# Kernel optimization log

Hardware: AMD Instinct MI355X
Metric: run time of the kernel (lower is better)

The kernel has to match this reference:

```python
import jax, jax.numpy as jnp
import numpy as np

N, E = 50000, 1600000
IN_DIM, HID, HEADS, DH, NCLS = 1280, 256, 4, 64, 6
NEG_SLOPE = 0.2
LN_EPS = 1e-5


def setup_inputs() -> dict:
    key = jax.random.key(0)
    ks = jax.random.split(key, 24)
    p = {}
    p['x'] = jax.random.normal(ks[0], (N, IN_DIM), dtype=jnp.float32)
    p['edge_index'] = jax.random.randint(ks[1], (2, E), 0, N, dtype=jnp.int64)
    s = 0.05
    p['W_in'] = jax.random.normal(ks[2], (IN_DIM, HID), dtype=jnp.float32) * s
    p['b_in'] = jnp.zeros((HID,), jnp.float32)
    for l in range(2):
        p[f'W_gat{l}'] = jax.random.normal(ks[3 + 6 * l], (HID, HEADS * DH), dtype=jnp.float32) * s
        p[f'att_src{l}'] = jax.random.normal(ks[4 + 6 * l], (HEADS, DH), dtype=jnp.float32) * s
        p[f'att_dst{l}'] = jax.random.normal(ks[5 + 6 * l], (HEADS, DH), dtype=jnp.float32) * s
        p[f'b_gat{l}'] = jnp.zeros((HEADS * DH,), jnp.float32)
        p[f'ln_g{l}'] = jnp.ones((HID,), jnp.float32)
        p[f'ln_b{l}'] = jnp.zeros((HID,), jnp.float32)
    p['W_c1'] = jax.random.normal(ks[20], (HID, HID // 2), dtype=jnp.float32) * s
    p['b_c1'] = jnp.zeros((HID // 2,), jnp.float32)
    p['W_c2'] = jax.random.normal(ks[21], (HID // 2, NCLS), dtype=jnp.float32) * s
    p['b_c2'] = jnp.zeros((NCLS,), jnp.float32)
    return p


def _layer_norm(h, g, b):
    mu = jnp.mean(h, axis=-1, keepdims=True)
    var = jnp.mean((h - mu) ** 2, axis=-1, keepdims=True)
    return (h - mu) * jax.lax.rsqrt(var + LN_EPS) * g + b


def _gat_conv(h, src, dst, W, a_src, a_dst, bias):
    # h: [N, HID] -> per-head projections [N, H, DH]
    xh = (h @ W).reshape(N, HEADS, DH)
    al_src = jnp.sum(xh * a_src, axis=-1)  # [N, H]
    al_dst = jnp.sum(xh * a_dst, axis=-1)  # [N, H]
    e = jax.nn.leaky_relu(al_src[src] + al_dst[dst], NEG_SLOPE)  # [E', H]
    # edge softmax over incoming edges of each destination node
    m = jax.ops.segment_max(e, dst, num_segments=N)
    e = jnp.exp(e - m[dst])
    denom = jax.ops.segment_sum(e, dst, num_segments=N)
    w = e / denom[dst]  # [E', H]
    msg = xh[src] * w[:, :, None]  # [E', H, DH]
    out = jax.ops.segment_sum(msg, dst, num_segments=N)  # [N, H, DH]
    return out.reshape(N, HEADS * DH) + bias


def reference(x, edge_index, W_in, b_in, W_gat0, att_src0, att_dst0, b_gat0, ln_g0, ln_b0,
              W_gat1, att_src1, att_dst1, b_gat1, ln_g1, ln_b1, W_c1, b_c1, W_c2, b_c2):
    # add self loops (PyG GATConv default)
    loop = jnp.arange(N, dtype=edge_index.dtype)
    src = jnp.concatenate([edge_index[0], loop])
    dst = jnp.concatenate([edge_index[1], loop])

    h = jax.nn.relu(x @ W_in + b_in)

    for (Wg, asrc, adst, bg, g, b) in ((W_gat0, att_src0, att_dst0, b_gat0, ln_g0, ln_b0),
                                       (W_gat1, att_src1, att_dst1, b_gat1, ln_g1, ln_b1)):
        h_new = _gat_conv(h, src, dst, Wg, asrc, adst, bg)
        h_new = jax.nn.relu(_layer_norm(h_new, g, b))
        h = h + h_new

    logits = jax.nn.relu(h @ W_c1 + b_c1) @ W_c2 + b_c2
    return logits
```

## Files before the change

### kernel.cpp

```cpp
#include <hip/hip_runtime.h>

#define NN 50000
#define EE 1600000
#define INDIM 1280
#define HID 256
#define HEADS 4
#define DHD 64
#define NCLS 6
#define NEG 0.2f
#define LNEPS 1e-5f

typedef __attribute__((ext_vector_type(8))) short short8;
typedef __attribute__((ext_vector_type(4))) float floatx4;

__device__ __forceinline__ unsigned short f2b(float f) {
    unsigned int u = __float_as_uint(f);
    u += 0x7FFF + ((u >> 16) & 1);
    return (unsigned short)(u >> 16);
}
__device__ __forceinline__ float b2f(unsigned short b) {
    return __uint_as_float(((unsigned int)b) << 16);
}

__global__ void init_cnt_kernel(int* __restrict__ cnt) {
    int n = blockIdx.x * 256 + threadIdx.x;
    if (n < NN) cnt[n] = 1;
}

__global__ void count_edges_kernel(const int* __restrict__ dst, int* __restrict__ cnt) {
    int e = blockIdx.x * 256 + threadIdx.x;
    if (e < EE) atomicAdd(&cnt[dst[e]], 1);
}

__global__ __launch_bounds__(1024) void scan1_kernel(const int* __restrict__ cnt,
                                                     int* __restrict__ scanned,
                                                     int* __restrict__ chtot, int n) {
    __shared__ int wsum[16];
    int tid = threadIdx.x, lane = tid & 63, wv = tid >> 6;
    int i = blockIdx.x * 1024 + tid;
    int s = (i < n) ? cnt[i] : 0;
#pragma unroll
    for (int off = 1; off < 64; off <<= 1) {
        int t = __shfl_up(s, off, 64);
        if (lane >= off) s += t;
    }
    if (lane == 63) wsum[wv] = s;
    __syncthreads();
    if (tid < 16) {
        int ws = wsum[tid];
#pragma unroll
        for (int off = 1; off < 16; off <<= 1) {
            int t = __shfl_up(ws, off, 16);
            if (tid >= off) ws += t;
        }
        wsum[tid] = ws;
    }
    __syncthreads();
    s += (wv > 0) ? wsum[wv - 1] : 0;
    if (i < n) scanned[i] = s;
    if (tid == 1023) chtot[blockIdx.x] = s;
}

__global__ void scan2_kernel(int* __restrict__ chtot, int nch) {
    int lane = threadIdx.x;
    int v = (lane < nch) ? chtot[lane] : 0;
#pragma unroll
    for (int off = 1; off < 64; off <<= 1) {
        int t = __shfl_up(v, off, 64);
        if (lane >= off) v += t;
    }
    if (lane < nch) chtot[lane] = v;
}

__global__ void scan3_kernel(const int* __restrict__ scanned, const int* __restrict__ chtot,
                             int* __restrict__ rowptr, int n) {
    int i = blockIdx.x * 256 + threadIdx.x;
    if (i == 0) rowptr[0] = 0;
    if (i < n) {
        int ch = i >> 10;
        rowptr[i + 1] = scanned[i] + (ch ? chtot[ch - 1] : 0);
    }
}

__global__ void copyfill_kernel(const int* __restrict__ rowptr, int* __restrict__ cursor,
                                int* __restrict__ csr) {
    int n = blockIdx.x * 256 + threadIdx.x;
    if (n < NN) {
        int p = rowptr[n];
        csr[p] = n;
        cursor[n] = p + 1;
    }
}

__global__ void scatter_edges_kernel(const int* __restrict__ src, const int* __restrict__ dst,
                                     int* __restrict__ cursor, int* __restrict__ csr) {
    int e = blockIdx.x * 256 + threadIdx.x;
    if (e < EE) {
        int d = dst[e];
        int pos = atomicAdd(&cursor[d], 1);
        csr[pos] = src[e];
    }
}

__global__ void transpose_w_kernel(const float* __restrict__ W, unsigned short* __restrict__ WT,
                                   int K, int N) {
    int idx = blockIdx.x * 256 + threadIdx.x;
    if (idx >= K * N) return;
    int n = idx / K, k = idx % K;
    WT[idx] = f2b(W[(size_t)k * N + n]);
}

template <int AF32, int ACT, int WF32, int WB16>
__global__ __launch_bounds__(256) void mgemm_kernel(const float* __restrict__ Af,
                                                    const unsigned short* __restrict__ Ab,
                                                    const unsigned short* __restrict__ BT,
                                                    const float* __restrict__ bias,
                                                    float* __restrict__ Cf,
                                                    unsigned short* __restrict__ Cb,
                                                    int M, int K, int N) {
    __shared__ __align__(16) unsigned short Als[16 * 512];
    __shared__ __align__(16) unsigned short Bls[8 * 512];
    int tid = threadIdx.x;
    int wv = tid >> 6, ln = tid & 63;
    int n0 = blockIdx.x * 64, m0 = blockIdx.y * 128;

    floatx4 acc[2][4] = {};

    for (int k0 = 0; k0 < K; k0 += 64) {
#pragma unroll
        for (int i = 0; i < 4; i++) {
            int e = tid + i * 256;
            int r = e >> 3, c8 = e & 7;
            int gm = m0 + r;
            int4 v = {0, 0, 0, 0};
            if (gm < M) {
                if (AF32) {
                    const float* s = Af + (size_t)gm * K + k0 + c8 * 8;
                    float4 f0 = *(const float4*)s;
                    float4 f1 = *(const float4*)(s + 4);
                    unsigned short u[8] = {f2b(f0.x), f2b(f0.y), f2b(f0.z), f2b(f0.w),
                                           f2b(f1.x), f2b(f1.y), f2b(f1.z), f2b(f1.w)};
                    v = *(const int4*)u;
                } else {
                    v = *(const int4*)(Ab + (size_t)gm * K + k0 + c8 * 8);
                }
            }
            int blk = (r >> 4) * 2 + (c8 >> 2);
            int lslot = (r & 15) + 16 * (c8 & 3);
            *(int4*)&Als[blk * 512 + lslot * 8] = v;
        }
#pragma unroll
        for (int i = 0; i < 2; i++) {
            int e = tid + i * 256;
            int r = e >> 3, c8 = e & 7;
            int4 v = *(const int4*)(BT + (size_t)(n0 + r) * K + k0 + c8 * 8);
            int blk = (r >> 4) * 2 + (c8 >> 2);
            int lslot = (r & 15) + 16 * (c8 & 3);
            *(int4*)&Bls[blk * 512 + lslot * 8] = v;
        }
        __syncthreads();
#pragma unroll
        for (int ks = 0; ks < 2; ks++) {
            short8 a0 = *(const short8*)&Als[((wv * 2 + 0) * 2 + ks) * 512 + ln * 8];
            short8 a1 = *(const short8*)&Als[((wv * 2 + 1) * 2 + ks) * 512 + ln * 8];
#pragma unroll
            for (int nt = 0; nt < 4; nt++) {
                short8 b = *(const short8*)&Bls[(nt * 2 + ks) * 512 + ln * 8];
                acc[0][nt] = __builtin_amdgcn_mfma_f32_16x16x32_bf16(a0, b, acc[0][nt], 0, 0, 0);
                acc[1][nt] = __builtin_amdgcn_mfma_f32_16x16x32_bf16(a1, b, acc[1][nt], 0, 0, 0);
            }
        }
        __syncthreads();
    }

#pragma unroll
    for (int ms = 0; ms < 2; ms++) {
#pragma unroll
        for (int nt = 0; nt < 4; nt++) {
            int col = n0 + nt * 16 + (ln & 15);
            int rb = m0 + (wv * 2 + ms) * 16 + (ln >> 4) * 4;
            float bi = bias ? bias[col] : 0.f;
#pragma unroll
            for (int r = 0; r < 4; r++) {
                int row = rb + r;
                if (row < M) {
                    float v = acc[ms][nt][r] + bi;
                    if (ACT) v = fmaxf(v, 0.f);
                    if (WF32) Cf[(size_t)row * N + col] = v;
                    if (WB16) Cb[(size_t)row * N + col] = f2b(v);
                }
            }
        }
    }
}

template <int AF32, int ACT, int WF32, int WB16>
__global__ __launch_bounds__(256) void mgemm_n256_kernel(const float* __restrict__ Af,
                                                         const unsigned short* __restrict__ Ab,
                                                         const unsigned short* __restrict__ BT,
                                                         const float* __restrict__ bias,
                                                         float* __restrict__ Cf,
                                                         unsigned short* __restrict__ Cb,
                                                         int M, int K) {
    __shared__ __align__(16) unsigned short Als[8 * 512];
    __shared__ __align__(16) unsigned short Bls[32 * 512];
    int tid = threadIdx.x;
    int wv = tid >> 6, ln = tid & 63;
    int m0 = blockIdx.x * 64;

    floatx4 acc[4][4] = {};

    for (int k0 = 0; k0 < K; k0 += 64) {
#pragma unroll
        for (int i = 0; i < 2; i++) {
            int e = tid + i * 256;
            int r = e >> 3, c8 = e & 7;
            int gm = m0 + r;
            int4 v = {0, 0, 0, 0};
            if (gm < M) {
                if (AF32) {
                    const float* s = Af + (size_t)gm * K + k0 + c8 * 8;
                    float4 f0 = *(const float4*)s;
                    float4 f1 = *(const float4*)(s + 4);
                    unsigned short u[8] = {f2b(f0.x), f2b(f0.y), f2b(f0.z), f2b(f0.w),
                                           f2b(f1.x), f2b(f1.y), f2b(f1.z), f2b(f1.w)};
                    v = *(const int4*)u;
                } else {
                    v = *(const int4*)(Ab + (size_t)gm * K + k0 + c8 * 8);
                }
            }
            int blk = (r >> 4) * 2 + (c8 >> 2);
            int lslot = (r & 15) + 16 * (c8 & 3);
            *(int4*)&Als[blk * 512 + lslot * 8] = v;
        }
#pragma unroll
        for (int i = 0; i < 8; i++) {
            int e = tid + i * 256;
            int r = e >> 3, c8 = e & 7;
            int4 v = *(const int4*)(BT + (size_t)r * K + k0 + c8 * 8);
            int blk = (r >> 4) * 2 + (c8 >> 2);
            int lslot = (r & 15) + 16 * (c8 & 3);
            *(int4*)&Bls[blk * 512 + lslot * 8] = v;
        }
        __syncthreads();
#pragma unroll
        for (int ks = 0; ks < 2; ks++) {
            short8 am[4];
#pragma unroll
            for (int mt = 0; mt < 4; mt++)
                am[mt] = *(const short8*)&Als[(mt * 2 + ks) * 512 + ln * 8];
#pragma unroll
            for (int nt4 = 0; nt4 < 4; nt4++) {
                int nt = wv * 4 + nt4;
                short8 b = *(const short8*)&Bls[(nt * 2 + ks) * 512 + ln * 8];
#pragma unroll
                for (int mt = 0; mt < 4; mt++)
                    acc[mt][nt4] = __builtin_amdgcn_mfma_f32_16x16x32_bf16(am[mt], b, acc[mt][nt4], 0, 0, 0);
            }
        }
        __syncthreads();
    }

#pragma unroll
    for (int mt = 0; mt < 4; mt++) {
#pragma unroll
        for (int nt4 = 0; nt4 < 4; nt4++) {
            int col = wv * 64 + nt4 * 16 + (ln & 15);
            int rb = m0 + mt * 16 + (ln >> 4) * 4;
            float bi = bias ? bias[col] : 0.f;
#pragma unroll
            for (int r = 0; r < 4; r++) {
                int row = rb + r;
                if (row < M) {
                    float v = acc[mt][nt4][r] + bi;
                    if (ACT) v = fmaxf(v, 0.f);
                    if (WF32) Cf[(size_t)row * HID + col] = v;
                    if (WB16) Cb[(size_t)row * HID + col] = f2b(v);
                }
            }
        }
    }
}

__global__ __launch_bounds__(256) void proj_al_kernel(const unsigned short* __restrict__ xhb,
                                                      const float* __restrict__ a_src,
                                                      const float* __restrict__ a_dst,
                                                      float* __restrict__ al_s,
                                                      float* __restrict__ al_d) {
    int n = blockIdx.x * 4 + (threadIdx.x >> 6);
    if (n >= NN) return;
    int lane = threadIdx.x & 63;
    ushort4 v4 = ((const ushort4*)(xhb + (size_t)n * HID))[lane];
    int base = lane * 4;
    float4 as4 = *(const float4*)&a_src[base];
    float4 ad4 = *(const float4*)&a_dst[base];
    float x0 = b2f(v4.x), x1 = b2f(v4.y), x2 = b2f(v4.z), x3 = b2f(v4.w);
    float ps = x0 * as4.x + x1 * as4.y + x2 * as4.z + x3 * as4.w;
    float pd = x0 * ad4.x + x1 * ad4.y + x2 * ad4.z + x3 * ad4.w;
#pragma unroll
    for (int off = 8; off > 0; off >>= 1) {
        ps += __shfl_down(ps, off, 16);
        pd += __shfl_down(pd, off, 16);
    }
    if ((lane & 15) == 0) {
        int h = lane >> 4;
        al_s[n * 4 + h] = ps;
        al_d[n * 4 + h] = pd;
    }
}

__global__ __launch_bounds__(256) void agg_ln_kernel(const int* __restrict__ rowptr,
                                                     const int* __restrict__ csr,
                                                     const float* __restrict__ al_s,
                                                     const float* __restrict__ al_d,
                                                     const unsigned short* __restrict__ xhb,
                                                     const float* __restrict__ bgat,
                                                     const float* __restrict__ g,
                                                     const float* __restrict__ bb,
                                                     float* __restrict__ h,
                                                     unsigned short* __restrict__ hb) {
    int wv = threadIdx.x >> 6, ln = threadIdx.x & 63;
    int n = blockIdx.x * 4 + wv;
    if (n >= NN) return;
    int start = rowptr[n], end = rowptr[n + 1];
    float4 ad = *(const float4*)&al_d[n * 4];

    float d0 = 0.f, d1 = 0.f, d2 = 0.f, d3 = 0.f;
    for (int i = start + ln; i < end; i += 64) {
        int s = csr[i];
        float4 as = *(const float4*)&al_s[s * 4];
        float e0 = as.x + ad.x; e0 = e0 > 0.f ? e0 : NEG * e0;
        float e1 = as.y + ad.y; e1 = e1 > 0.f ? e1 : NEG * e1;
        float e2 = as.z + ad.z; e2 = e2 > 0.f ? e2 : NEG * e2;
        float e3 = as.w + ad.w; e3 = e3 > 0.f ? e3 : NEG * e3;
        d0 += __expf(e0); d1 += __expf(e1); d2 += __expf(e2); d3 += __expf(e3);
    }
#pragma unroll
    for (int off = 32; off > 0; off >>= 1) {
        d0 += __shfl_xor(d0, off, 64);
        d1 += __shfl_xor(d1, off, 64);
        d2 += __shfl_xor(d2, off, 64);
        d3 += __shfl_xor(d3, off, 64);
    }
    int myh = ln >> 4;
    float invh = 1.f / ((myh == 0) ? d0 : (myh == 1) ? d1 : (myh == 2) ? d2 : d3);
    float adh = (myh == 0) ? ad.x : (myh == 1) ? ad.y : (myh == 2) ? ad.z : ad.w;

    float a0 = 0.f, a1 = 0.f, a2 = 0.f, a3 = 0.f;
#pragma unroll 2
    for (int i = start; i < end; i++) {
        int s = csr[i];
        float e = al_s[s * 4 + myh] + adh;
        e = e > 0.f ? e : NEG * e;
        float w = __expf(e) * invh;
        ushort4 mv = *(const ushort4*)&xhb[(size_t)s * HID + ln * 4];
        a0 = fmaf(w, b2f(mv.x), a0);
        a1 = fmaf(w, b2f(mv.y), a1);
        a2 = fmaf(w, b2f(mv.z), a2);
        a3 = fmaf(w, b2f(mv.w), a3);
    }

    float4 bg = *(const float4*)&bgat[ln * 4];
    float v0 = a0 + bg.x, v1 = a1 + bg.y, v2 = a2 + bg.z, v3 = a3 + bg.w;
    float ps = v0 + v1 + v2 + v3;
    float ps2 = v0 * v0 + v1 * v1 + v2 * v2 + v3 * v3;
#pragma unroll
    for (int off = 32; off > 0; off >>= 1) {
        ps += __shfl_xor(ps, off, 64);
        ps2 += __shfl_xor(ps2, off, 64);
    }
    float mu = ps * (1.f / HID);
    float var = ps2 * (1.f / HID) - mu * mu;
    float rs = rsqrtf(var + LNEPS);
    float4 gg = *(const float4*)&g[ln * 4];
    float4 bbv = *(const float4*)&bb[ln * 4];
    float o0 = fmaxf((v0 - mu) * rs * gg.x + bbv.x, 0.f);
    float o1 = fmaxf((v1 - mu) * rs * gg.y + bbv.y, 0.f);
    float o2 = fmaxf((v2 - mu) * rs * gg.z + bbv.z, 0.f);
    float o3 = fmaxf((v3 - mu) * rs * gg.w + bbv.w, 0.f);
    size_t idx = (size_t)n * HID + ln * 4;
    float4 hv = *(const float4*)&h[idx];
    float4 nh = make_float4(hv.x + o0, hv.y + o1, hv.z + o2, hv.w + o3);
    *(float4*)&h[idx] = nh;
    ushort4 nb = {f2b(nh.x), f2b(nh.y), f2b(nh.z), f2b(nh.w)};
    *(ushort4*)&hb[idx] = nb;
}

__global__ void cls2_kernel(const float* __restrict__ mid, const float* __restrict__ W,
                            const float* __restrict__ bias, float* __restrict__ out) {
    int idx = blockIdx.x * 256 + threadIdx.x;
    if (idx >= NN * NCLS) return;
    int n = idx / NCLS, c = idx % NCLS;
    const float* row = mid + (size_t)n * (HID / 2);
    float acc = bias[c];
#pragma unroll 8
    for (int k = 0; k < HID / 2; k++) acc += row[k] * W[k * NCLS + c];
    out[idx] = acc;
}

extern "C" void kernel_launch(void* const* d_in, const int* in_sizes, int n_in,
                              void* d_out, int out_size, void* d_ws, size_t ws_size,
                              hipStream_t stream) {
    const float* x    = (const float*)d_in[0];
    const int*   ei   = (const int*)d_in[1];
    const float* W_in = (const float*)d_in[2];
    const float* b_in = (const float*)d_in[3];
    const float* W_gat[2]   = {(const float*)d_in[4],  (const float*)d_in[10]};
    const float* att_src[2] = {(const float*)d_in[5],  (const float*)d_in[11]};
    const float* att_dst[2] = {(const float*)d_in[6],  (const float*)d_in[12]};
    const float* b_gat[2]   = {(const float*)d_in[7],  (const float*)d_in[13]};
    const float* ln_g[2]    = {(const float*)d_in[8],  (const float*)d_in[14]};
    const float* ln_b[2]    = {(const float*)d_in[9],  (const float*)d_in[15]};
    const float* W_c1 = (const float*)d_in[16];
    const float* b_c1 = (const float*)d_in[17];
    const float* W_c2 = (const float*)d_in[18];
    const float* b_c2 = (const float*)d_in[19];

    char* ws = (char*)d_ws;
    size_t off = 0;
    auto alloc = [&](size_t bytes) -> void* {
        void* p = ws + off;
        off += (bytes + 255) & ~(size_t)255;
        return p;
    };
    float*          h   = (float*)alloc((size_t)NN * HID * 4);
    unsigned short* hb  = (unsigned short*)alloc((size_t)NN * HID * 2);
    unsigned short* xhb = (unsigned short*)alloc((size_t)NN * HID * 2);
    float* al_s = (float*)alloc((size_t)NN * HEADS * 4);
    float* al_d = (float*)alloc((size_t)NN * HEADS * 4);
    int* rowptr  = (int*)alloc((size_t)(NN + 1) * 4);
    int* cursor  = (int*)alloc((size_t)NN * 4);
    int* csr     = (int*)alloc((size_t)(EE + NN) * 4);
    int* scanned = (int*)alloc((size_t)NN * 4);
    int* chtot   = (int*)alloc(64 * 4);
    unsigned short* WinT = (unsigned short*)alloc((size_t)HID * INDIM * 2);
    unsigned short* WgT0 = (unsigned short*)alloc((size_t)HID * HID * 2);
    unsigned short* WgT1 = (unsigned short*)alloc((size_t)HID * HID * 2);
    unsigned short* Wc1T = (unsigned short*)alloc((size_t)(HID / 2) * HID * 2);
    unsigned short* WgT[2] = {WgT0, WgT1};
    float* mid = (float*)xhb;

    const int* srcv = ei;
    const int* dstv = ei + EE;

    transpose_w_kernel<<<(INDIM * HID + 255) / 256, 256, 0, stream>>>(W_in, WinT, INDIM, HID);
    transpose_w_kernel<<<(HID * HID + 255) / 256, 256, 0, stream>>>(W_gat[0], WgT0, HID, HID);
    transpose_w_kernel<<<(HID * HID + 255) / 256, 256, 0, stream>>>(W_gat[1], WgT1, HID, HID);
    transpose_w_kernel<<<(HID * (HID / 2) + 255) / 256, 256, 0, stream>>>(W_c1, Wc1T, HID, HID / 2);

    int nch = (NN + 1023) / 1024;
    init_cnt_kernel<<<(NN + 255) / 256, 256, 0, stream>>>(cursor);
    count_edges_kernel<<<(EE + 255) / 256, 256, 0, stream>>>(dstv, cursor);
    scan1_kernel<<<nch, 1024, 0, stream>>>(cursor, scanned, chtot, NN);
    scan2_kernel<<<1, 64, 0, stream>>>(chtot, nch);
    scan3_kernel<<<(NN + 255) / 256, 256, 0, stream>>>(scanned, chtot, rowptr, NN);
    copyfill_kernel<<<(NN + 255) / 256, 256, 0, stream>>>(rowptr, cursor, csr);
    scatter_edges_kernel<<<(EE + 255) / 256, 256, 0, stream>>>(srcv, dstv, cursor, csr);

    int MB64 = (NN + 63) / 64;

    mgemm_n256_kernel<1, 1, 1, 1><<<MB64, 256, 0, stream>>>(
        x, nullptr, WinT, b_in, h, hb, NN, INDIM);

    for (int l = 0; l < 2; l++) {
        mgemm_n256_kernel<0, 0, 0, 1><<<MB64, 256, 0, stream>>>(
            nullptr, hb, WgT[l], nullptr, nullptr, xhb, NN, HID);
        proj_al_kernel<<<(NN + 3) / 4, 256, 0, stream>>>(xhb, att_src[l], att_dst[l], al_s, al_d);
        agg_ln_kernel<<<(NN + 3) / 4, 256, 0, stream>>>(rowptr, csr, al_s, al_d, xhb,
                                                        b_gat[l], ln_g[l], ln_b[l], h, hb);
    }

    mgemm_kernel<0, 1, 1, 0><<<dim3((HID / 2) / 64, (NN + 127) / 128), 256, 0, stream>>>(
        nullptr, hb, Wc1T, b_c1, mid, nullptr, NN, HID, HID / 2);
    cls2_kernel<<<(NN * NCLS + 255) / 256, 256, 0, stream>>>(mid, W_c2, b_c2, (float*)d_out);
}
```

Measured before the change: 1.110 ms.

## Prepack weights into MFMA fragment layout and drop LDS staging in GEMMs

Weights are packed once into the exact per-lane MFMA fragment order, so the GEMM kernels load A and B operands straight from global memory into registers with no shared-memory staging and no __syncthreads. The three GEMM variants are merged into one templated kernel, and the classifier GEMM now uses 64-row blocks covering all 128 columns. The aim is to remove LDS round-trips and barriers. In exchange, each wave re-reads the A rows from global memory or cache instead of sharing them through LDS, and the A loads are strided by row, which may hurt coalescing on the large 1280-wide input GEMM.

After: 1.162 ms. 4.7% more time.

```diff
diff --git a/kernel.cpp b/kernel.cpp
--- a/kernel.cpp
+++ b/kernel.cpp
@@ -102,180 +102,94 @@
     }
 }
 
-__global__ void transpose_w_kernel(const float* __restrict__ W, unsigned short* __restrict__ WT,
-                                   int K, int N) {
+__global__ void pack_w_kernel(const float* __restrict__ W, unsigned short* __restrict__ out,
+                              int K, int N) {
     int idx = blockIdx.x * 256 + threadIdx.x;
-    if (idx >= K * N) return;
-    int n = idx / K, k = idx % K;
-    WT[idx] = f2b(W[(size_t)k * N + n]);
-}
-
-template <int AF32, int ACT, int WF32, int WB16>
-__global__ __launch_bounds__(256) void mgemm_kernel(const float* __restrict__ Af,
+    int total = (K >> 6) * (N >> 4) * 2 * 64;
+    if (idx >= total) return;
+    int ln = idx & 63;
+    int t = idx >> 6;
+    int ks = t & 1; t >>= 1;
+    int NT = N >> 4;
+    int nt = t % NT, kc = t / NT;
+    int n = nt * 16 + (ln & 15);
+    int k = kc * 64 + ks * 32 + ((ln >> 4) << 3);
+    unsigned short u[8];
+#pragma unroll
+    for (int j = 0; j < 8; j++) u[j] = f2b(W[(size_t)(k + j) * N + n]);
+    *(int4*)&out[(size_t)idx * 8] = *(const int4*)u;
+}
+
+template <int AF32, int NT, int ACT, int WF32, int WB16>
+__global__ __launch_bounds__(256) void fgemm_kernel(const float* __restrict__ Af,
                                                     const unsigned short* __restrict__ Ab,
-                                                    const unsigned short* __restrict__ BT,
+                                                    const unsigned short* __restrict__ Bf,
                                                     const float* __restrict__ bias,
                                                     float* __restrict__ Cf,
                                                     unsigned short* __restrict__ Cb,
-                                                    int M, int K, int N) {
-    __shared__ __align__(16) unsigned short Als[16 * 512];
-    __shared__ __align__(16) unsigned short Bls[8 * 512];
-    int tid = threadIdx.x;
-    int wv = tid >> 6, ln = tid & 63;
-    int n0 = blockIdx.x * 64, m0 = blockIdx.y * 128;
-
-    floatx4 acc[2][4] = {};
+                                                    int M, int K) {
+    constexpr int NW = NT / 4;
+    int wv = threadIdx.x >> 6, ln = threadIdx.x & 63;
+    int m0 = blockIdx.x * 64;
+    int kcol = (ln >> 4) << 3;
+
+    size_t arow[4];
+#pragma unroll
+    for (int mt = 0; mt < 4; mt++) {
+        int r = m0 + mt * 16 + (ln & 15);
+        arow[mt] = (size_t)min(r, M - 1) * K;
+    }
+
+    floatx4 acc[4][NW] = {};
 
     for (int k0 = 0; k0 < K; k0 += 64) {
 #pragma unroll
-        for (int i = 0; i < 4; i++) {
-            int e = tid + i * 256;
-            int r = e >> 3, c8 = e & 7;
-            int gm = m0 + r;
-            int4 v = {0, 0, 0, 0};
-            if (gm < M) {
+        for (int ks = 0; ks < 2; ks++) {
+            int kb = k0 + ks * 32 + kcol;
+            short8 a[4];
+#pragma unroll
+            for (int mt = 0; mt < 4; mt++) {
                 if (AF32) {
-                    const float* s = Af + (size_t)gm * K + k0 + c8 * 8;
+                    const float* s = Af + arow[mt] + kb;
                     float4 f0 = *(const float4*)s;
                     float4 f1 = *(const float4*)(s + 4);
                     unsigned short u[8] = {f2b(f0.x), f2b(f0.y), f2b(f0.z), f2b(f0.w),
                                            f2b(f1.x), f2b(f1.y), f2b(f1.z), f2b(f1.w)};
-                    v = *(const int4*)u;
+                    a[mt] = *(const short8*)u;
                 } else {
-                    v = *(const int4*)(Ab + (size_t)gm * K + k0 + c8 * 8);
+                    a[mt] = *(const short8*)(Ab + arow[mt] + kb);
                 }
             }
-            int blk = (r >> 4) * 2 + (c8 >> 2);
-            int lslot = (r & 15) + 16 * (c8 & 3);
-            *(int4*)&Als[blk * 512 + lslot * 8] = v;
+            short8 b[NW];
+#pragma unroll
+            for (int nw = 0; nw < NW; nw++) {
+                size_t boff = ((((size_t)(k0 >> 6) * NT + (wv * NW + nw)) * 2 + ks) * 64 + ln) * 8;
+                b[nw] = *(const short8*)(Bf + boff);
+            }
+#pragma unroll
+            for (int nw = 0; nw < NW; nw++)
+#pragma unroll
+                for (int mt = 0; mt < 4; mt++)
+                    acc[mt][nw] = __builtin_amdgcn_mfma_f32_16x16x32_bf16(a[mt], b[nw], acc[mt][nw], 0, 0, 0);
         }
-#pragma unroll
-        for (int i = 0; i < 2; i++) {
-            int e = tid + i * 256;
-            int r = e >> 3, c8 = e & 7;
-            int4 v = *(const int4*)(BT + (size_t)(n0 + r) * K + k0 + c8 * 8);
-            int blk = (r >> 4) * 2 + (c8 >> 2);
-            int lslot = (r & 15) + 16 * (c8 & 3);
-            *(int4*)&Bls[blk * 512 + lslot * 8] = v;
-        }
-        __syncthreads();
-#pragma unroll
-        for (int ks = 0; ks < 2; ks++) {
-            short8 a0 = *(const short8*)&Als[((wv * 2 + 0) * 2 + ks) * 512 + ln * 8];
-            short8 a1 = *(const short8*)&Als[((wv * 2 + 1) * 2 + ks) * 512 + ln * 8];
-#pragma unroll
-            for (int nt = 0; nt < 4; nt++) {
-                short8 b = *(const short8*)&Bls[(nt * 2 + ks) * 512 + ln * 8];
-                acc[0][nt] = __builtin_amdgcn_mfma_f32_16x16x32_bf16(a0, b, acc[0][nt], 0, 0, 0);
-                acc[1][nt] = __builtin_amdgcn_mfma_f32_16x16x32_bf16(a1, b, acc[1][nt], 0, 0, 0);
-            }
-        }
-        __syncthreads();
-    }
-
-#pragma unroll
-    for (int ms = 0; ms < 2; ms++) {
-#pragma unroll
-        for (int nt = 0; nt < 4; nt++) {
-            int col = n0 + nt * 16 + (ln & 15);
-            int rb = m0 + (wv * 2 + ms) * 16 + (ln >> 4) * 4;
+    }
+
+    const int Nout = NT * 16;
+#pragma unroll
+    for (int mt = 0; mt < 4; mt++) {
+#pragma unroll
+        for (int nw = 0; nw < NW; nw++) {
+            int col = (wv * NW + nw) * 16 + (ln & 15);
+            int rb = m0 + mt * 16 + (ln >> 4) * 4;
             float bi = bias ? bias[col] : 0.f;
 #pragma unroll
             for (int r = 0; r < 4; r++) {
                 int row = rb + r;
                 if (row < M) {
-                    float v = acc[ms][nt][r] + bi;
+                    float v = acc[mt][nw][r] + bi;
                     if (ACT) v = fmaxf(v, 0.f);
-                    if (WF32) Cf[(size_t)row * N + col] = v;
-                    if (WB16) Cb[(size_t)row * N + col] = f2b(v);
-                }
-            }
-        }
-    }
-}
-
-template <int AF32, int ACT, int WF32, int WB16>
-__global__ __launch_bounds__(256) void mgemm_n256_kernel(const float* __restrict__ Af,
-                                                         const unsigned short* __restrict__ Ab,
-                                                         const unsigned short* __restrict__ BT,
-                                                         const float* __restrict__ bias,
-                                                         float* __restrict__ Cf,
-                                                         unsigned short* __restrict__ Cb,
-                                                         int M, int K) {
-    __shared__ __align__(16) unsigned short Als[8 * 512];
-    __shared__ __align__(16) unsigned short Bls[32 * 512];
-    int tid = threadIdx.x;
-    int wv = tid >> 6, ln = tid & 63;
-    int m0 = blockIdx.x * 64;
-
-    floatx4 acc[4][4] = {};
-
-    for (int k0 = 0; k0 < K; k0 += 64) {
-#pragma unroll
-        for (int i = 0; i < 2; i++) {
-            int e = tid + i * 256;
-            int r = e >> 3, c8 = e & 7;
-            int gm = m0 + r;
-            int4 v = {0, 0, 0, 0};
-            if (gm < M) {
-                if (AF32) {
-                    const float* s = Af + (size_t)gm * K + k0 + c8 * 8;
-                    float4 f0 = *(const float4*)s;
-                    float4 f1 = *(const float4*)(s + 4);
-                    unsigned short u[8] = {f2b(f0.x), f2b(f0.y), f2b(f0.z), f2b(f0.w),
-                                           f2b(f1.x), f2b(f1.y), f2b(f1.z), f2b(f1.w)};
-                    v = *(const int4*)u;
-                } else {
-                    v = *(const int4*)(Ab + (size_t)gm * K + k0 + c8 * 8);
-                }
-            }
-            int blk = (r >> 4) * 2 + (c8 >> 2);
-            int lslot = (r & 15) + 16 * (c8 & 3);
-            *(int4*)&Als[blk * 512 + lslot * 8] = v;
-        }
-#pragma unroll
-        for (int i = 0; i < 8; i++) {
-            int e = tid + i * 256;
-            int r = e >> 3, c8 = e & 7;
-            int4 v = *(const int4*)(BT + (size_t)r * K + k0 + c8 * 8);
-            int blk = (r >> 4) * 2 + (c8 >> 2);
-            int lslot = (r & 15) + 16 * (c8 & 3);
-            *(int4*)&Bls[blk * 512 + lslot * 8] = v;
-        }
-        __syncthreads();
-#pragma unroll
-        for (int ks = 0; ks < 2; ks++) {
-            short8 am[4];
-#pragma unroll
-            for (int mt = 0; mt < 4; mt++)
-                am[mt] = *(const short8*)&Als[(mt * 2 + ks) * 512 + ln * 8];
-#pragma unroll
-            for (int nt4 = 0; nt4 < 4; nt4++) {
-                int nt = wv * 4 + nt4;
-                short8 b = *(const short8*)&Bls[(nt * 2 + ks) * 512 + ln * 8];
-#pragma unroll
-                for (int mt = 0; mt < 4; mt++)
-                    acc[mt][nt4] = __builtin_amdgcn_mfma_f32_16x16x32_bf16(am[mt], b, acc[mt][nt4], 0, 0, 0);
-            }
-        }
-        __syncthreads();
-    }
-
-#pragma unroll
-    for (int mt = 0; mt < 4; mt++) {
-#pragma unroll
-        for (int nt4 = 0; nt4 < 4; nt4++) {
-            int col = wv * 64 + nt4 * 16 + (ln & 15);
-            int rb = m0 + mt * 16 + (ln >> 4) * 4;
-            float bi = bias ? bias[col] : 0.f;
-#pragma unroll
-            for (int r = 0; r < 4; r++) {
-                int row = rb + r;
-                if (row < M) {
-                    float v = acc[mt][nt4][r] + bi;
-                    if (ACT) v = fmaxf(v, 0.f);
-                    if (WF32) Cf[(size_t)row * HID + col] = v;
-                    if (WB16) Cb[(size_t)row * HID + col] = f2b(v);
+                    if (WF32) Cf[(size_t)row * Nout + col] = v;
+                    if (WB16) Cb[(size_t)row * Nout + col] = f2b(v);
                 }
             }
         }
@@ -433,20 +347,20 @@
     int* csr     = (int*)alloc((size_t)(EE + NN) * 4);
     int* scanned = (int*)alloc((size_t)NN * 4);
     int* chtot   = (int*)alloc(64 * 4);
-    unsigned short* WinT = (unsigned short*)alloc((size_t)HID * INDIM * 2);
-    unsigned short* WgT0 = (unsigned short*)alloc((size_t)HID * HID * 2);
-    unsigned short* WgT1 = (unsigned short*)alloc((size_t)HID * HID * 2);
-    unsigned short* Wc1T = (unsigned short*)alloc((size_t)(HID / 2) * HID * 2);
-    unsigned short* WgT[2] = {WgT0, WgT1};
+    unsigned short* WinF = (unsigned short*)alloc((size_t)HID * INDIM * 2);
+    unsigned short* WgF0 = (unsigned short*)alloc((size_t)HID * HID * 2);
+    unsigned short* WgF1 = (unsigned short*)alloc((size_t)HID * HID * 2);
+    unsigned short* Wc1F = (unsigned short*)alloc((size_t)(HID / 2) * HID * 2);
+    unsigned short* WgF[2] = {WgF0, WgF1};
     float* mid = (float*)xhb;
 
     const int* srcv = ei;
     const int* dstv = ei + EE;
 
-    transpose_w_kernel<<<(INDIM * HID + 255) / 256, 256, 0, stream>>>(W_in, WinT, INDIM, HID);
-    transpose_w_kernel<<<(HID * HID + 255) / 256, 256, 0, stream>>>(W_gat[0], WgT0, HID, HID);
-    transpose_w_kernel<<<(HID * HID + 255) / 256, 256, 0, stream>>>(W_gat[1], WgT1, HID, HID);
-    transpose_w_kernel<<<(HID * (HID / 2) + 255) / 256, 256, 0, stream>>>(W_c1, Wc1T, HID, HID / 2);
+    pack_w_kernel<<<(INDIM * HID / 8 + 255) / 256, 256, 0, stream>>>(W_in, WinF, INDIM, HID);
+    pack_w_kernel<<<(HID * HID / 8 + 255) / 256, 256, 0, stream>>>(W_gat[0], WgF0, HID, HID);
+    pack_w_kernel<<<(HID * HID / 8 + 255) / 256, 256, 0, stream>>>(W_gat[1], WgF1, HID, HID);
+    pack_w_kernel<<<(HID * (HID / 2) / 8 + 255) / 256, 256, 0, stream>>>(W_c1, Wc1F, HID, HID / 2);
 
     int nch = (NN + 1023) / 1024;
     init_cnt_kernel<<<(NN + 255) / 256, 256, 0, stream>>>(cursor);
@@ -459,18 +373,18 @@
 
     int MB64 = (NN + 63) / 64;
 
-    mgemm_n256_kernel<1, 1, 1, 1><<<MB64, 256, 0, stream>>>(
-        x, nullptr, WinT, b_in, h, hb, NN, INDIM);
+    fgemm_kernel<1, 16, 1, 1, 1><<<MB64, 256, 0, stream>>>(
+        x, nullptr, WinF, b_in, h, hb, NN, INDIM);
 
     for (int l = 0; l < 2; l++) {
-        mgemm_n256_kernel<0, 0, 0, 1><<<MB64, 256, 0, stream>>>(
-            nullptr, hb, WgT[l], nullptr, nullptr, xhb, NN, HID);
+        fgemm_kernel<0, 16, 0, 0, 1><<<MB64, 256, 0, stream>>>(
+            nullptr, hb, WgF[l], nullptr, nullptr, xhb, NN, HID);
         proj_al_kernel<<<(NN + 3) / 4, 256, 0, stream>>>(xhb, att_src[l], att_dst[l], al_s, al_d);
         agg_ln_kernel<<<(NN + 3) / 4, 256, 0, stream>>>(rowptr, csr, al_s, al_d, xhb,
                                                         b_gat[l], ln_g[l], ln_b[l], h, hb);
     }
 
-    mgemm_kernel<0, 1, 1, 0><<<dim3((HID / 2) / 64, (NN + 127) / 128), 256, 0, stream>>>(
-        nullptr, hb, Wc1T, b_c1, mid, nullptr, NN, HID, HID / 2);
+    fgemm_kernel<0, 8, 1, 1, 0><<<MB64, 256, 0, stream>>>(
+        nullptr, hb, Wc1F, b_c1, mid, nullptr, NN, HID);
     cls2_kernel<<<(NN * NCLS + 255) / 256, 256, 0, stream>>>(mid, W_c2, b_c2, (float*)d_out);
 }
```
